# Kernel tuning notes

Hardware: AMD Instinct MI355X
Metric: run time of the kernel (lower is better)

The kernel has to match this reference:

```python
import jax, jax.numpy as jnp
import numpy as np

N_KEEP = 256      # number of retained DCT coefficients per box
MASK_LEN = 128    # reconstructed square mask side (gt_mask_len)
TOPK = 50         # boxes kept per image


def _zigzag_order(n):
    # order[i] = flat index (r*n+c) where the i-th zigzag element lives (JPEG zigzag)
    order = []
    for s in range(2 * n - 1):
        if s % 2 == 0:
            rng = range(min(s, n - 1), max(0, s - n + 1) - 1, -1)
        else:
            rng = range(max(0, s - n + 1), min(s, n - 1) + 1)
        for r in rng:
            order.append(r * n + (s - r))
    return np.asarray(order, dtype=np.int64)


def _dct_matrix(n):
    # orthonormal DCT-II matrix D; cv2.idct(Y) == D.T @ Y @ D
    k = np.arange(n)[:, None].astype(np.float64)
    m = np.arange(n)[None, :].astype(np.float64)
    D = np.cos(np.pi * (2.0 * m + 1.0) * k / (2.0 * n)) * np.sqrt(2.0 / n)
    D[0] *= np.sqrt(0.5)
    return D.astype(np.float32)

_INV_ZZ = np.argsort(_zigzag_order(MASK_LEN))  # flat[j] = padded_vec[_INV_ZZ[j]]
_DCT = _dct_matrix(MASK_LEN)


def setup_inputs() -> dict:
    key = jax.random.key(0)
    ks = jax.random.split(key, 6)
    B, Q, C, A = 32, 300, 91, 10
    return {
        "out_logits": jax.random.normal(ks[0], (B, Q, C), jnp.float32),
        "out_bbox": jax.random.uniform(ks[1], (B, Q, 4), jnp.float32),
        "out_vector": jax.random.normal(ks[2], (B, Q, N_KEEP), jnp.float32),
        "out_interms": jax.random.normal(ks[3], (B, Q, C), jnp.float32),
        "out_actions": jax.random.normal(ks[4], (B, 1, A), jnp.float32),
        "target_sizes": jax.random.randint(ks[5], (B, 2), 480, 1333, jnp.int32),
    }


def _box_cxcywh_to_xyxy(b):
    cx, cy, w, h = jnp.split(b, 4, axis=-1)
    return jnp.concatenate([cx - 0.5 * w, cy - 0.5 * h, cx + 0.5 * w, cy + 0.5 * h], axis=-1)


def reference(out_logits, out_bbox, out_vector, out_interms, out_actions, target_sizes):
    B, Q, C = out_logits.shape
    prob = jax.nn.sigmoid(out_logits)
    topk_values, topk_indexes = jax.lax.top_k(prob.reshape(B, -1), TOPK)
    scores = topk_values
    topk_boxes = topk_indexes // C          # [B, TOPK] query ids
    labels = topk_indexes % C               # [B, TOPK]

    boxes = _box_cxcywh_to_xyxy(out_bbox)
    boxes = jnp.take_along_axis(boxes, topk_boxes[:, :, None], axis=1)  # [B, TOPK, 4]

    prob_interms = jax.nn.sigmoid(out_interms)
    si = jnp.take_along_axis(prob_interms, topk_boxes[:, :, None], axis=1)  # [B, TOPK, C_int]
    labels_interms = jnp.argmax(si, axis=2)
    scores_interms = jnp.max(si, axis=2)

    prob_actions = jax.nn.softmax(out_actions[:, 0, :], axis=1)
    labels_action = jnp.argmax(prob_actions, axis=1)

    vectors = jnp.take_along_axis(out_vector, topk_boxes[:, :, None], axis=1)  # [B, TOPK, N_KEEP]

    ts = target_sizes.astype(boxes.dtype)
    img_h, img_w = ts[:, 0], ts[:, 1]
    scale_fct = jnp.stack([img_w, img_h, img_w, img_h], axis=1)
    boxes = boxes * scale_fct[:, None, :]

    # --- batched inverse zigzag + 2D IDCT + midpoint threshold ---
    pad = MASK_LEN * MASK_LEN - N_KEEP
    padded = jnp.pad(vectors, ((0, 0), (0, 0), (0, pad)))           # [B,TOPK,L*L]
    flat = padded[..., jnp.asarray(_INV_ZZ)]                         # inverse zigzag (gather)
    blocks = flat.reshape(B, TOPK, MASK_LEN, MASK_LEN)
    D = jnp.asarray(_DCT)
    re_mask = jnp.einsum('kn,bqkl,lm->bqnm', D, blocks, D)           # cv2.idct per box
    mx = jnp.max(re_mask, axis=(-2, -1), keepdims=True)
    mn = jnp.min(re_mask, axis=(-2, -1), keepdims=True)
    masks = (re_mask > 0.5 * (mx + mn)).astype(jnp.float32)          # [B,TOPK,L,L]

    return (scores, labels, boxes, masks, scores_interms, labels_interms, labels_action)
```

## Files before the change

kernel.cpp:

```cpp
#include <hip/hip_runtime.h>
#include <math.h>

#define BB 32
#define QQ 300
#define CC 91
#define TOPK 50
#define NKEEP 256
#define ML 128
#define QC (QQ * CC)
#define QC4 (QC / 4)
#define NWAVE 16
#define NSLICE 8
#define SL4 854
#define CAP 2048

#define OFF_SCORES ((size_t)0)
#define OFF_LABELS ((size_t)1600)
#define OFF_BOXES  ((size_t)3200)
#define OFF_MASKS  ((size_t)9600)
#define OFF_SI     ((size_t)26224000)
#define OFF_LI     ((size_t)26225600)
#define OFF_LA     ((size_t)26227200)

__device__ __forceinline__ uint32_t fkey(float f) {
    uint32_t u = __float_as_uint(f);
    return (u >> 31) ? ~u : (u | 0x80000000u);
}

__device__ __forceinline__ void pick_boundary(const uint32_t* bins, int kth, int lane,
                                              uint32_t* sBin, int* sNeed, int* sCnt) {
    uint4 h4 = *(const uint4*)&bins[lane * 4];
    uint32_t s3 = h4.w;
    uint32_t s2 = h4.z + s3;
    uint32_t s1 = h4.y + s2;
    uint32_t s0 = h4.x + s1;
    uint32_t inc = s0;
#pragma unroll
    for (int off = 1; off < 64; off <<= 1) {
        uint32_t v = __shfl_down(inc, off);
        if (lane + off < 64) inc += v;
    }
    uint32_t higher = inc - s0;
    uint32_t sarr[4] = {s0, s1, s2, s3};
    uint32_t harr[4] = {h4.x, h4.y, h4.z, h4.w};
#pragma unroll
    for (int c = 0; c < 4; ++c) {
        int cge = (int)(sarr[c] + higher);
        int cgt = cge - (int)harr[c];
        if (cge >= kth && cgt < kth) {
            *sBin = (uint32_t)(lane * 4 + c);
            *sNeed = kth - cgt;
            *sCnt = (int)harr[c];
        }
    }
}

__global__ __launch_bounds__(256) void topk_hist(const float* __restrict__ logits,
                                                 float* __restrict__ wsD,
                                                 int* __restrict__ wsZZ,
                                                 uint32_t* __restrict__ wsH) {
    int s = blockIdx.x;
    int b = blockIdx.y;
    int t = threadIdx.x;

    if (b == 0) {
        int lo = s * 368, hi = lo + 368;
        if (hi > 23 * 128) hi = 23 * 128;
        for (int idx = lo + t; idx < hi; idx += 256) {
            int k = idx >> 7, m = idx & 127;
            double v = cos((M_PI * (2.0 * (double)m + 1.0) * (double)k) / 256.0) * 0.125;
            if (k == 0) v *= sqrt(0.5);
            wsD[idx] = (float)v;
        }
        if (s == 0) {
            int j = t;
            int ss = 0;
            while ((ss + 1) * (ss + 2) / 2 <= j) ++ss;
            int o = j - ss * (ss + 1) / 2;
            int r = (ss & 1) ? o : (ss - o);
            int c = ss - r;
            wsZZ[j] = (r << 5) | c;
        }
    }

    __shared__ uint32_t hw[4 * 256];
    for (int i = t; i < 4 * 256; i += 256) hw[i] = 0;
    __syncthreads();

    uint32_t* myh = &hw[(t >> 6) * 256];
    const float4* base4 = (const float4*)(logits + (size_t)b * QC);
    int lo4 = s * SL4;
    int hi4 = lo4 + SL4; if (hi4 > QC4) hi4 = QC4;
    for (int p4 = lo4 + t; p4 < hi4; p4 += 256) {
        float4 v = base4[p4];
        atomicAdd(&myh[fkey(v.x) >> 24], 1u);
        atomicAdd(&myh[fkey(v.y) >> 24], 1u);
        atomicAdd(&myh[fkey(v.z) >> 24], 1u);
        atomicAdd(&myh[fkey(v.w) >> 24], 1u);
    }
    __syncthreads();

    if (t < 256) {
        uint32_t sum = hw[t] + hw[256 + t] + hw[512 + t] + hw[768 + t];
        wsH[((size_t)(b * NSLICE + s)) * 256 + t] = sum;
    }
}

__global__ __launch_bounds__(1024) void topk_select(const float* __restrict__ logits,
                                                    const float* __restrict__ bbox,
                                                    const float* __restrict__ actions,
                                                    const int* __restrict__ tsz,
                                                    float* __restrict__ out,
                                                    int* __restrict__ wsQ,
                                                    const uint32_t* __restrict__ wsH) {
    int b = blockIdx.x;
    int t = threadIdx.x;
    int lane = t & 63, w = t >> 6;

    __shared__ uint32_t histw[NWAVE * 256];
    __shared__ __attribute__((aligned(16))) uint32_t h2[256];
    __shared__ __attribute__((aligned(16))) uint32_t scn[256];
    __shared__ uint32_t sP;
    __shared__ int      sNeed, sCnt;
    __shared__ uint32_t cKey[TOPK];
    __shared__ int      cIdx[TOPK];
    __shared__ int      cntTop, cntN, cntE, sMin;
    __shared__ uint32_t candK[2][CAP];
    __shared__ int      candI[2][CAP];

    const float4* base4 = (const float4*)(logits + (size_t)b * QC);

    if (t < 256) {
        uint32_t ssum = 0;
#pragma unroll
        for (int s = 0; s < NSLICE; ++s) ssum += wsH[((size_t)(b * NSLICE + s)) * 256 + t];
        scn[t] = ssum;
    }
    if (t == 0) { cntTop = 0; cntN = 0; cntE = 0; }
    __syncthreads();
    if (t < 64) pick_boundary(scn, TOPK, lane, &sP, &sNeed, &sCnt);
    __syncthreads();
    uint32_t P0 = sP << 24;
    int need = sNeed;
    int nC0 = sCnt;

    if (nC0 <= CAP) {
        for (int p4 = t; p4 < QC4; p4 += 1024) {
            float4 v = base4[p4];
            uint32_t kk[4] = {fkey(v.x), fkey(v.y), fkey(v.z), fkey(v.w)};
#pragma unroll
            for (int c = 0; c < 4; ++c) {
                uint32_t hb = kk[c] & 0xFF000000u;
                if (hb > P0) {
                    int pos = atomicAdd(&cntTop, 1);
                    cKey[pos] = kk[c]; cIdx[pos] = 4 * p4 + c;
                } else if (hb == P0) {
                    int pos = atomicAdd(&cntN, 1);
                    candK[0][pos] = kk[c]; candI[0][pos] = 4 * p4 + c;
                }
            }
        }
        __syncthreads();
        int nc = cntN;
        int cur = 0;

        for (int level = 1; level <= 3; ++level) {
            if (nc <= need) break;
            int shift = 24 - 8 * level;
            if (t < 256) h2[t] = 0;
            if (t == 0) cntN = 0;
            __syncthreads();
            for (int j2 = t; j2 < nc; j2 += 1024)
                atomicAdd(&h2[(candK[cur][j2] >> shift) & 255u], 1u);
            __syncthreads();
            if (t < 64) pick_boundary(h2, need, lane, &sP, &sNeed, &sCnt);
            __syncthreads();
            uint32_t sub = sP;
            int needN = sNeed;
            for (int j2 = t; j2 < nc; j2 += 1024) {
                uint32_t k2 = candK[cur][j2]; int i2 = candI[cur][j2];
                uint32_t sb = (k2 >> shift) & 255u;
                if (sb > sub) {
                    int pos = atomicAdd(&cntTop, 1);
                    cKey[pos] = k2; cIdx[pos] = i2;
                } else if (sb == sub) {
                    int pos = atomicAdd(&cntN, 1);
                    candK[cur ^ 1][pos] = k2; candI[cur ^ 1][pos] = i2;
                }
            }
            __syncthreads();
            nc = cntN; need = needN; cur ^= 1;
        }

        int base = cntTop;
        if (nc <= need) {
            for (int j2 = t; j2 < nc; j2 += 1024) {
                cKey[base + j2] = candK[cur][j2];
                cIdx[base + j2] = candI[cur][j2];
            }
        } else {
            for (int j2 = t; j2 < nc; j2 += 1024) {
                int my = candI[cur][j2];
                int rank = 0;
                for (int m = 0; m < nc; ++m) rank += (candI[cur][m] < my);
                if (rank < need) { cKey[base + rank] = candK[cur][j2]; cIdx[base + rank] = my; }
            }
        }
        __syncthreads();
    } else {
        uint32_t Pfull = P0;
        int kth = need;
        uint32_t* myh = &histw[w * 256];
        for (int pass = 1; pass < 4; ++pass) {
            int shift = 24 - 8 * pass;
            for (int i2 = t; i2 < NWAVE * 256; i2 += 1024) histw[i2] = 0;
            __syncthreads();
            uint32_t pmask = 0xFFFFFFFFu << (shift + 8);
            for (int p4 = t; p4 < QC4; p4 += 1024) {
                float4 v = base4[p4];
                uint32_t kk[4] = {fkey(v.x), fkey(v.y), fkey(v.z), fkey(v.w)};
#pragma unroll
                for (int c = 0; c < 4; ++c)
                    if ((kk[c] & pmask) == Pfull) atomicAdd(&myh[(kk[c] >> shift) & 255u], 1u);
            }
            __syncthreads();
            if (t < 256) {
                uint32_t ssum = 0;
#pragma unroll
                for (int ww = 0; ww < NWAVE; ++ww) ssum += histw[ww * 256 + t];
                scn[t] = ssum;
            }
            __syncthreads();
            if (t < 64) pick_boundary(scn, kth, lane, &sP, &sNeed, &sCnt);
            __syncthreads();
            Pfull |= (sP << shift);
            kth = sNeed;
        }
        if (t == 0) { cntTop = 0; cntE = 0; }
        __syncthreads();
        for (int p4 = t; p4 < QC4; p4 += 1024) {
            float4 v = base4[p4];
            uint32_t kk[4] = {fkey(v.x), fkey(v.y), fkey(v.z), fkey(v.w)};
#pragma unroll
            for (int c = 0; c < 4; ++c) {
                if (kk[c] > Pfull) {
                    int pos = atomicAdd(&cntTop, 1);
                    cKey[pos] = kk[c]; cIdx[pos] = 4 * p4 + c;
                } else if (kk[c] == Pfull) {
                    int pos = atomicAdd(&cntE, 1);
                    if (pos < CAP) candI[0][pos] = 4 * p4 + c;
                }
            }
        }
        __syncthreads();
        int cgt2 = cntTop;
        int ne = cntE;
        if (ne <= CAP) {
            for (int j2 = t; j2 < ne; j2 += 1024) {
                int my = candI[0][j2];
                int rank = 0;
                for (int m = 0; m < ne; ++m) rank += (candI[0][m] < my);
                if (rank < kth) { cKey[cgt2 + rank] = Pfull; cIdx[cgt2 + rank] = my; }
            }
            __syncthreads();
        } else {
            int prevMin = -1;
            for (int r = 0; r < kth; ++r) {
                if (t == 0) sMin = 0x7fffffff;
                __syncthreads();
                int loc = 0x7fffffff;
                for (int p4 = t; p4 < QC4; p4 += 1024) {
                    float4 v = base4[p4];
                    uint32_t kk[4] = {fkey(v.x), fkey(v.y), fkey(v.z), fkey(v.w)};
#pragma unroll
                    for (int c = 0; c < 4; ++c) {
                        int idx = 4 * p4 + c;
                        if (kk[c] == Pfull && idx > prevMin) loc = min(loc, idx);
                    }
                }
                atomicMin(&sMin, loc);
                __syncthreads();
                prevMin = sMin;
                if (t == 0) { cKey[cgt2 + r] = Pfull; cIdx[cgt2 + r] = prevMin; }
                __syncthreads();
            }
        }
    }

    if (t < TOPK) {
        uint32_t myk = cKey[t]; int myi = cIdx[t];
        int rank = 0;
        for (int m = 0; m < TOPK; ++m) {
            uint32_t ok = cKey[m]; int oi = cIdx[m];
            rank += (ok > myk) || (ok == myk && oi < myi);
        }
        uint32_t u = (myk >> 31) ? (myk & 0x7fffffffu) : ~myk;
        float val = __uint_as_float(u);
        int q = myi / CC;
        int label = myi - q * CC;
        out[OFF_SCORES + b * TOPK + rank] = 1.0f / (1.0f + expf(-val));
        out[OFF_LABELS + b * TOPK + rank] = (float)label;
        wsQ[b * TOPK + rank] = q;
        const float* bbp = bbox + ((size_t)(b * QQ + q)) * 4;
        float cx = bbp[0], cy = bbp[1], bw = bbp[2], bh = bbp[3];
        float ih = (float)tsz[b * 2 + 0];
        float iw = (float)tsz[b * 2 + 1];
        float* bo = out + OFF_BOXES + ((size_t)(b * TOPK + rank)) * 4;
        bo[0] = (cx - 0.5f * bw) * iw;
        bo[1] = (cy - 0.5f * bh) * ih;
        bo[2] = (cx + 0.5f * bw) * iw;
        bo[3] = (cy + 0.5f * bh) * ih;
    }
    if (t == 0) {
        const float* ap = actions + (size_t)b * 10;
        float bv = ap[0]; int bi = 0;
        for (int i = 1; i < 10; ++i) { if (ap[i] > bv) { bv = ap[i]; bi = i; } }
        out[OFF_LA + b] = (float)bi;
    }
}

__global__ __launch_bounds__(256) void mask_kernel(const float* __restrict__ vec,
                                                   const float* __restrict__ interms,
                                                   const int* __restrict__ wsQ,
                                                   const float* __restrict__ wsD,
                                                   const int* __restrict__ wsZZ,
                                                   float* __restrict__ out) {
    int j = blockIdx.x;
    int b = blockIdx.y;
    int t = threadIdx.x;

    __shared__ float sT[23 * 128];
    __shared__ float sB[23 * 24];
    __shared__ float redv[4];
    __shared__ int   redi[4];
    __shared__ float redmn[4], redmx[4];

    int q = wsQ[b * TOPK + j];

    for (int i = t; i < 23 * 24; i += 256) sB[i] = 0.0f;
    __syncthreads();

    {
        int kl = wsZZ[t];
        float x = vec[((size_t)(b * QQ + q)) * NKEEP + t];
        sB[(kl >> 5) * 24 + (kl & 31)] = x;
    }

    int lane = t & 63, w = t >> 6;
    {
        float x = (t < CC) ? interms[((size_t)(b * QQ + q)) * CC + t] : -INFINITY;
        int xi = (t < CC) ? t : 0x7fffffff;
#pragma unroll
        for (int off = 32; off >= 1; off >>= 1) {
            float ov = __shfl_down(x, off);
            int   oi = __shfl_down(xi, off);
            bool better = (ov > x) || (ov == x && oi < xi);
            x = better ? ov : x;
            xi = better ? oi : xi;
        }
        if (lane == 0) { redv[w] = x; redi[w] = xi; }
    }
    __syncthreads();

    if (t == 0) {
        float gv = redv[0]; int gi = redi[0];
        for (int k = 1; k < 4; ++k) {
            bool better = (redv[k] > gv) || (redv[k] == gv && redi[k] < gi);
            gv = better ? redv[k] : gv;
            gi = better ? redi[k] : gi;
        }
        out[OFF_SI + (size_t)b * TOPK + j] = 1.0f / (1.0f + expf(-gv));
        out[OFF_LI + (size_t)b * TOPK + j] = (float)gi;
    }

    {
        int n = t & 127, h = t >> 7;
        float Dn[23];
#pragma unroll
        for (int k = 0; k < 23; ++k) Dn[k] = wsD[k * 128 + n];
#define S1L(L) { float a1 = 0.0f; \
    _Pragma("unroll") \
    for (int k = 0; k <= 22 - (L); ++k) a1 += Dn[k] * sB[k * 24 + (L)]; \
    sT[(L) * 128 + n] = a1; }
        if (h == 0) {
            S1L(0) S1L(2) S1L(4) S1L(6) S1L(8) S1L(10)
            S1L(12) S1L(14) S1L(16) S1L(18) S1L(20) S1L(22)
        } else {
            S1L(1) S1L(3) S1L(5) S1L(7) S1L(9) S1L(11)
            S1L(13) S1L(15) S1L(17) S1L(19) S1L(21)
        }
#undef S1L
    }
    __syncthreads();

    int tr = t >> 4, tc = t & 15;
    float acc[8][8];
#pragma unroll
    for (int a = 0; a < 8; ++a)
#pragma unroll
        for (int c = 0; c < 8; ++c) acc[a][c] = 0.0f;

#pragma unroll 4
    for (int l = 0; l < 23; ++l) {
        const float4 Ta = *(const float4*)&sT[l * 128 + tr * 8];
        const float4 Tb = *(const float4*)&sT[l * 128 + tr * 8 + 4];
        const float4 Da = *(const float4*)&wsD[l * 128 + tc * 8];
        const float4 Db = *(const float4*)&wsD[l * 128 + tc * 8 + 4];
        float Tv[8] = {Ta.x, Ta.y, Ta.z, Ta.w, Tb.x, Tb.y, Tb.z, Tb.w};
        float Dv[8] = {Da.x, Da.y, Da.z, Da.w, Db.x, Db.y, Db.z, Db.w};
#pragma unroll
        for (int a = 0; a < 8; ++a)
#pragma unroll
            for (int c = 0; c < 8; ++c) acc[a][c] += Tv[a] * Dv[c];
    }

    float mn = acc[0][0], mx = acc[0][0];
#pragma unroll
    for (int a = 0; a < 8; ++a)
#pragma unroll
        for (int c = 0; c < 8; ++c) {
            mn = fminf(mn, acc[a][c]);
            mx = fmaxf(mx, acc[a][c]);
        }
#pragma unroll
    for (int off = 32; off >= 1; off >>= 1) {
        mn = fminf(mn, __shfl_down(mn, off));
        mx = fmaxf(mx, __shfl_down(mx, off));
    }
    if (lane == 0) { redmn[w] = mn; redmx[w] = mx; }
    __syncthreads();
    float gmn = fminf(fminf(redmn[0], redmn[1]), fminf(redmn[2], redmn[3]));
    float gmx = fmaxf(fmaxf(redmx[0], redmx[1]), fmaxf(redmx[2], redmx[3]));
    float thr = 0.5f * (gmx + gmn);

    size_t bse = OFF_MASKS + ((size_t)(b * TOPK + j)) * 16384 + (size_t)tc * 8;
#pragma unroll
    for (int a = 0; a < 8; ++a) {
        int n = tr * 8 + a;
        float4 w0 = make_float4(acc[a][0] > thr ? 1.0f : 0.0f,
                                acc[a][1] > thr ? 1.0f : 0.0f,
                                acc[a][2] > thr ? 1.0f : 0.0f,
                                acc[a][3] > thr ? 1.0f : 0.0f);
        float4 w1 = make_float4(acc[a][4] > thr ? 1.0f : 0.0f,
                                acc[a][5] > thr ? 1.0f : 0.0f,
                                acc[a][6] > thr ? 1.0f : 0.0f,
                                acc[a][7] > thr ? 1.0f : 0.0f);
        *(float4*)&out[bse + (size_t)n * 128]     = w0;
        *(float4*)&out[bse + (size_t)n * 128 + 4] = w1;
    }
}

extern "C" void kernel_launch(void* const* d_in, const int* in_sizes, int n_in,
                              void* d_out, int out_size, void* d_ws, size_t ws_size,
                              hipStream_t stream) {
    const float* logits  = (const float*)d_in[0];
    const float* bbox    = (const float*)d_in[1];
    const float* vec     = (const float*)d_in[2];
    const float* interms = (const float*)d_in[3];
    const float* actions = (const float*)d_in[4];
    const int*   tsz     = (const int*)d_in[5];
    float* out = (float*)d_out;

    float*    wsD  = (float*)d_ws;
    int*      wsZZ = (int*)(wsD + 2944);
    int*      wsQ  = wsZZ + 256;
    uint32_t* wsH  = (uint32_t*)(wsQ + 1600);

    hipLaunchKernelGGL(topk_hist, dim3(NSLICE, BB), dim3(256), 0, stream,
                       logits, wsD, wsZZ, wsH);
    hipLaunchKernelGGL(topk_select, dim3(BB), dim3(1024), 0, stream,
                       logits, bbox, actions, tsz, out, wsQ, wsH);
    hipLaunchKernelGGL(mask_kernel, dim3(TOPK, BB), dim3(256), 0, stream,
                       vec, interms, wsQ, wsD, wsZZ, out);
}
```

Baseline: 163.3 us.

## Fuse top-k selection and mask reconstruction into one kernel with redundant per-block selection

Replaces the three-kernel pipeline (histogram, select, mask) with a single kernel launched over (TOPK, B). Every block redundantly recomputes the full top-k selection for its image and keeps only the entry whose rank equals its block index. The DCT table and zigzag map are now built in shared memory per block instead of read from workspace, and shared memory is reused through a union. This removes two launch boundaries and the global workspace round-trips. In exchange, the 109K-element logit scan and radix selection are repeated 50 times per image with only 256 threads per block, and the candidate capacity shrinks, so the slower fallback path may be taken more often.

```diff
diff --git a/kernel.cpp b/kernel.cpp
--- a/kernel.cpp
+++ b/kernel.cpp
@@ -6,13 +6,10 @@
 #define CC 91
 #define TOPK 50
 #define NKEEP 256
-#define ML 128
 #define QC (QQ * CC)
 #define QC4 (QC / 4)
-#define NWAVE 16
-#define NSLICE 8
-#define SL4 854
-#define CAP 2048
+#define NT 256
+#define CAP 1024
 
 #define OFF_SCORES ((size_t)0)
 #define OFF_LABELS ((size_t)1600)
@@ -55,97 +52,68 @@
     }
 }
 
-__global__ __launch_bounds__(256) void topk_hist(const float* __restrict__ logits,
-                                                 float* __restrict__ wsD,
-                                                 int* __restrict__ wsZZ,
-                                                 uint32_t* __restrict__ wsH) {
-    int s = blockIdx.x;
+union alignas(16) Smem {
+    struct {
+        uint32_t hw[4 * 256];
+        uint32_t scn[256];
+        uint32_t h2[256];
+        uint32_t candK[2][CAP];
+        int      candI[2][CAP];
+        uint32_t cKey[TOPK];
+        int      cIdx[TOPK];
+    } s;
+    struct {
+        float sD[23 * 128];
+        float sT[23 * 128];
+        float sB[23 * 24];
+        int   sZZ[256];
+        float redv[4]; int redi[4];
+        float redmn[4], redmx[4];
+    } m;
+};
+
+__global__ __launch_bounds__(NT) void fused_all(const float* __restrict__ logits,
+                                                const float* __restrict__ bbox,
+                                                const float* __restrict__ vec,
+                                                const float* __restrict__ interms,
+                                                const float* __restrict__ actions,
+                                                const int* __restrict__ tsz,
+                                                float* __restrict__ out) {
+    int j = blockIdx.x;
     int b = blockIdx.y;
     int t = threadIdx.x;
-
-    if (b == 0) {
-        int lo = s * 368, hi = lo + 368;
-        if (hi > 23 * 128) hi = 23 * 128;
-        for (int idx = lo + t; idx < hi; idx += 256) {
-            int k = idx >> 7, m = idx & 127;
-            double v = cos((M_PI * (2.0 * (double)m + 1.0) * (double)k) / 256.0) * 0.125;
-            if (k == 0) v *= sqrt(0.5);
-            wsD[idx] = (float)v;
-        }
-        if (s == 0) {
-            int j = t;
-            int ss = 0;
-            while ((ss + 1) * (ss + 2) / 2 <= j) ++ss;
-            int o = j - ss * (ss + 1) / 2;
-            int r = (ss & 1) ? o : (ss - o);
-            int c = ss - r;
-            wsZZ[j] = (r << 5) | c;
-        }
-    }
-
-    __shared__ uint32_t hw[4 * 256];
-    for (int i = t; i < 4 * 256; i += 256) hw[i] = 0;
-    __syncthreads();
-
-    uint32_t* myh = &hw[(t >> 6) * 256];
+    int lane = t & 63, w4 = t >> 6;
+
+    __shared__ Smem sm;
+    __shared__ uint32_t sP;
+    __shared__ int sNeed, sCnt, cntTop, cntN, cntE, sMin, sQ;
+
     const float4* base4 = (const float4*)(logits + (size_t)b * QC);
-    int lo4 = s * SL4;
-    int hi4 = lo4 + SL4; if (hi4 > QC4) hi4 = QC4;
-    for (int p4 = lo4 + t; p4 < hi4; p4 += 256) {
-        float4 v = base4[p4];
-        atomicAdd(&myh[fkey(v.x) >> 24], 1u);
-        atomicAdd(&myh[fkey(v.y) >> 24], 1u);
-        atomicAdd(&myh[fkey(v.z) >> 24], 1u);
-        atomicAdd(&myh[fkey(v.w) >> 24], 1u);
-    }
-    __syncthreads();
-
-    if (t < 256) {
-        uint32_t sum = hw[t] + hw[256 + t] + hw[512 + t] + hw[768 + t];
-        wsH[((size_t)(b * NSLICE + s)) * 256 + t] = sum;
-    }
-}
-
-__global__ __launch_bounds__(1024) void topk_select(const float* __restrict__ logits,
-                                                    const float* __restrict__ bbox,
-                                                    const float* __restrict__ actions,
-                                                    const int* __restrict__ tsz,
-                                                    float* __restrict__ out,
-                                                    int* __restrict__ wsQ,
-                                                    const uint32_t* __restrict__ wsH) {
-    int b = blockIdx.x;
-    int t = threadIdx.x;
-    int lane = t & 63, w = t >> 6;
-
-    __shared__ uint32_t histw[NWAVE * 256];
-    __shared__ __attribute__((aligned(16))) uint32_t h2[256];
-    __shared__ __attribute__((aligned(16))) uint32_t scn[256];
-    __shared__ uint32_t sP;
-    __shared__ int      sNeed, sCnt;
-    __shared__ uint32_t cKey[TOPK];
-    __shared__ int      cIdx[TOPK];
-    __shared__ int      cntTop, cntN, cntE, sMin;
-    __shared__ uint32_t candK[2][CAP];
-    __shared__ int      candI[2][CAP];
-
-    const float4* base4 = (const float4*)(logits + (size_t)b * QC);
-
-    if (t < 256) {
-        uint32_t ssum = 0;
-#pragma unroll
-        for (int s = 0; s < NSLICE; ++s) ssum += wsH[((size_t)(b * NSLICE + s)) * 256 + t];
-        scn[t] = ssum;
-    }
+
+    for (int i = t; i < 4 * 256; i += NT) sm.s.hw[i] = 0;
+    __syncthreads();
+    {
+        uint32_t* myh = &sm.s.hw[w4 * 256];
+        for (int p4 = t; p4 < QC4; p4 += NT) {
+            float4 v = base4[p4];
+            atomicAdd(&myh[fkey(v.x) >> 24], 1u);
+            atomicAdd(&myh[fkey(v.y) >> 24], 1u);
+            atomicAdd(&myh[fkey(v.z) >> 24], 1u);
+            atomicAdd(&myh[fkey(v.w) >> 24], 1u);
+        }
+    }
+    __syncthreads();
+    if (t < 256) sm.s.scn[t] = sm.s.hw[t] + sm.s.hw[256 + t] + sm.s.hw[512 + t] + sm.s.hw[768 + t];
     if (t == 0) { cntTop = 0; cntN = 0; cntE = 0; }
     __syncthreads();
-    if (t < 64) pick_boundary(scn, TOPK, lane, &sP, &sNeed, &sCnt);
+    if (t < 64) pick_boundary(sm.s.scn, TOPK, lane, &sP, &sNeed, &sCnt);
     __syncthreads();
     uint32_t P0 = sP << 24;
     int need = sNeed;
     int nC0 = sCnt;
 
     if (nC0 <= CAP) {
-        for (int p4 = t; p4 < QC4; p4 += 1024) {
+        for (int p4 = t; p4 < QC4; p4 += NT) {
             float4 v = base4[p4];
             uint32_t kk[4] = {fkey(v.x), fkey(v.y), fkey(v.z), fkey(v.w)};
 #pragma unroll
@@ -153,39 +121,38 @@
                 uint32_t hb = kk[c] & 0xFF000000u;
                 if (hb > P0) {
                     int pos = atomicAdd(&cntTop, 1);
-                    cKey[pos] = kk[c]; cIdx[pos] = 4 * p4 + c;
+                    sm.s.cKey[pos] = kk[c]; sm.s.cIdx[pos] = 4 * p4 + c;
                 } else if (hb == P0) {
                     int pos = atomicAdd(&cntN, 1);
-                    candK[0][pos] = kk[c]; candI[0][pos] = 4 * p4 + c;
+                    sm.s.candK[0][pos] = kk[c]; sm.s.candI[0][pos] = 4 * p4 + c;
                 }
             }
         }
         __syncthreads();
-        int nc = cntN;
-        int cur = 0;
+        int nc = cntN, cur = 0;
 
         for (int level = 1; level <= 3; ++level) {
             if (nc <= need) break;
             int shift = 24 - 8 * level;
-            if (t < 256) h2[t] = 0;
+            if (t < 256) sm.s.h2[t] = 0;
             if (t == 0) cntN = 0;
             __syncthreads();
-            for (int j2 = t; j2 < nc; j2 += 1024)
-                atomicAdd(&h2[(candK[cur][j2] >> shift) & 255u], 1u);
-            __syncthreads();
-            if (t < 64) pick_boundary(h2, need, lane, &sP, &sNeed, &sCnt);
+            for (int j2 = t; j2 < nc; j2 += NT)
+                atomicAdd(&sm.s.h2[(sm.s.candK[cur][j2] >> shift) & 255u], 1u);
+            __syncthreads();
+            if (t < 64) pick_boundary(sm.s.h2, need, lane, &sP, &sNeed, &sCnt);
             __syncthreads();
             uint32_t sub = sP;
             int needN = sNeed;
-            for (int j2 = t; j2 < nc; j2 += 1024) {
-                uint32_t k2 = candK[cur][j2]; int i2 = candI[cur][j2];
+            for (int j2 = t; j2 < nc; j2 += NT) {
+                uint32_t k2 = sm.s.candK[cur][j2]; int i2 = sm.s.candI[cur][j2];
                 uint32_t sb = (k2 >> shift) & 255u;
                 if (sb > sub) {
                     int pos = atomicAdd(&cntTop, 1);
-                    cKey[pos] = k2; cIdx[pos] = i2;
+                    sm.s.cKey[pos] = k2; sm.s.cIdx[pos] = i2;
                 } else if (sb == sub) {
                     int pos = atomicAdd(&cntN, 1);
-                    candK[cur ^ 1][pos] = k2; candI[cur ^ 1][pos] = i2;
+                    sm.s.candK[cur ^ 1][pos] = k2; sm.s.candI[cur ^ 1][pos] = i2;
                 }
             }
             __syncthreads();
@@ -194,29 +161,29 @@
 
         int base = cntTop;
         if (nc <= need) {
-            for (int j2 = t; j2 < nc; j2 += 1024) {
-                cKey[base + j2] = candK[cur][j2];
-                cIdx[base + j2] = candI[cur][j2];
+            for (int j2 = t; j2 < nc; j2 += NT) {
+                sm.s.cKey[base + j2] = sm.s.candK[cur][j2];
+                sm.s.cIdx[base + j2] = sm.s.candI[cur][j2];
             }
         } else {
-            for (int j2 = t; j2 < nc; j2 += 1024) {
-                int my = candI[cur][j2];
+            for (int j2 = t; j2 < nc; j2 += NT) {
+                int my = sm.s.candI[cur][j2];
                 int rank = 0;
-                for (int m = 0; m < nc; ++m) rank += (candI[cur][m] < my);
-                if (rank < need) { cKey[base + rank] = candK[cur][j2]; cIdx[base + rank] = my; }
+                for (int m = 0; m < nc; ++m) rank += (sm.s.candI[cur][m] < my);
+                if (rank < need) { sm.s.cKey[base + rank] = sm.s.candK[cur][j2]; sm.s.cIdx[base + rank] = my; }
             }
         }
         __syncthreads();
     } else {
         uint32_t Pfull = P0;
         int kth = need;
-        uint32_t* myh = &histw[w * 256];
+        uint32_t* myh = &sm.s.hw[w4 * 256];
         for (int pass = 1; pass < 4; ++pass) {
             int shift = 24 - 8 * pass;
-            for (int i2 = t; i2 < NWAVE * 256; i2 += 1024) histw[i2] = 0;
+            for (int i2 = t; i2 < 4 * 256; i2 += NT) sm.s.hw[i2] = 0;
             __syncthreads();
             uint32_t pmask = 0xFFFFFFFFu << (shift + 8);
-            for (int p4 = t; p4 < QC4; p4 += 1024) {
+            for (int p4 = t; p4 < QC4; p4 += NT) {
                 float4 v = base4[p4];
                 uint32_t kk[4] = {fkey(v.x), fkey(v.y), fkey(v.z), fkey(v.w)};
 #pragma unroll
@@ -224,31 +191,26 @@
                     if ((kk[c] & pmask) == Pfull) atomicAdd(&myh[(kk[c] >> shift) & 255u], 1u);
             }
             __syncthreads();
-            if (t < 256) {
-                uint32_t ssum = 0;
-#pragma unroll
-                for (int ww = 0; ww < NWAVE; ++ww) ssum += histw[ww * 256 + t];
-                scn[t] = ssum;
-            }
-            __syncthreads();
-            if (t < 64) pick_boundary(scn, kth, lane, &sP, &sNeed, &sCnt);
+            if (t < 256) sm.s.scn[t] = sm.s.hw[t] + sm.s.hw[256 + t] + sm.s.hw[512 + t] + sm.s.hw[768 + t];
+            __syncthreads();
+            if (t < 64) pick_boundary(sm.s.scn, kth, lane, &sP, &sNeed, &sCnt);
             __syncthreads();
             Pfull |= (sP << shift);
             kth = sNeed;
         }
         if (t == 0) { cntTop = 0; cntE = 0; }
         __syncthreads();
-        for (int p4 = t; p4 < QC4; p4 += 1024) {
+        for (int p4 = t; p4 < QC4; p4 += NT) {
             float4 v = base4[p4];
             uint32_t kk[4] = {fkey(v.x), fkey(v.y), fkey(v.z), fkey(v.w)};
 #pragma unroll
             for (int c = 0; c < 4; ++c) {
                 if (kk[c] > Pfull) {
                     int pos = atomicAdd(&cntTop, 1);
-                    cKey[pos] = kk[c]; cIdx[pos] = 4 * p4 + c;
+                    sm.s.cKey[pos] = kk[c]; sm.s.cIdx[pos] = 4 * p4 + c;
                 } else if (kk[c] == Pfull) {
                     int pos = atomicAdd(&cntE, 1);
-                    if (pos < CAP) candI[0][pos] = 4 * p4 + c;
+                    if (pos < CAP) sm.s.candI[0][pos] = 4 * p4 + c;
                 }
             }
         }
@@ -256,11 +218,11 @@
         int cgt2 = cntTop;
         int ne = cntE;
         if (ne <= CAP) {
-            for (int j2 = t; j2 < ne; j2 += 1024) {
-                int my = candI[0][j2];
+            for (int j2 = t; j2 < ne; j2 += NT) {
+                int my = sm.s.candI[0][j2];
                 int rank = 0;
-                for (int m = 0; m < ne; ++m) rank += (candI[0][m] < my);
-                if (rank < kth) { cKey[cgt2 + rank] = Pfull; cIdx[cgt2 + rank] = my; }
+                for (int m = 0; m < ne; ++m) rank += (sm.s.candI[0][m] < my);
+                if (rank < kth) { sm.s.cKey[cgt2 + rank] = Pfull; sm.s.cIdx[cgt2 + rank] = my; }
             }
             __syncthreads();
         } else {
@@ -269,7 +231,7 @@
                 if (t == 0) sMin = 0x7fffffff;
                 __syncthreads();
                 int loc = 0x7fffffff;
-                for (int p4 = t; p4 < QC4; p4 += 1024) {
+                for (int p4 = t; p4 < QC4; p4 += NT) {
                     float4 v = base4[p4];
                     uint32_t kk[4] = {fkey(v.x), fkey(v.y), fkey(v.z), fkey(v.w)};
 #pragma unroll
@@ -281,72 +243,71 @@
                 atomicMin(&sMin, loc);
                 __syncthreads();
                 prevMin = sMin;
-                if (t == 0) { cKey[cgt2 + r] = Pfull; cIdx[cgt2 + r] = prevMin; }
+                if (t == 0) { sm.s.cKey[cgt2 + r] = Pfull; sm.s.cIdx[cgt2 + r] = prevMin; }
                 __syncthreads();
             }
         }
     }
 
     if (t < TOPK) {
-        uint32_t myk = cKey[t]; int myi = cIdx[t];
+        uint32_t myk = sm.s.cKey[t]; int myi = sm.s.cIdx[t];
         int rank = 0;
         for (int m = 0; m < TOPK; ++m) {
-            uint32_t ok = cKey[m]; int oi = cIdx[m];
+            uint32_t ok = sm.s.cKey[m]; int oi = sm.s.cIdx[m];
             rank += (ok > myk) || (ok == myk && oi < myi);
         }
-        uint32_t u = (myk >> 31) ? (myk & 0x7fffffffu) : ~myk;
-        float val = __uint_as_float(u);
-        int q = myi / CC;
-        int label = myi - q * CC;
-        out[OFF_SCORES + b * TOPK + rank] = 1.0f / (1.0f + expf(-val));
-        out[OFF_LABELS + b * TOPK + rank] = (float)label;
-        wsQ[b * TOPK + rank] = q;
-        const float* bbp = bbox + ((size_t)(b * QQ + q)) * 4;
-        float cx = bbp[0], cy = bbp[1], bw = bbp[2], bh = bbp[3];
-        float ih = (float)tsz[b * 2 + 0];
-        float iw = (float)tsz[b * 2 + 1];
-        float* bo = out + OFF_BOXES + ((size_t)(b * TOPK + rank)) * 4;
-        bo[0] = (cx - 0.5f * bw) * iw;
-        bo[1] = (cy - 0.5f * bh) * ih;
-        bo[2] = (cx + 0.5f * bw) * iw;
-        bo[3] = (cy + 0.5f * bh) * ih;
-    }
-    if (t == 0) {
+        if (rank == j) {
+            uint32_t u = (myk >> 31) ? (myk & 0x7fffffffu) : ~myk;
+            float val = __uint_as_float(u);
+            int q = myi / CC;
+            int label = myi - q * CC;
+            out[OFF_SCORES + b * TOPK + j] = 1.0f / (1.0f + expf(-val));
+            out[OFF_LABELS + b * TOPK + j] = (float)label;
+            const float* bbp = bbox + ((size_t)(b * QQ + q)) * 4;
+            float cx = bbp[0], cy = bbp[1], bw = bbp[2], bh = bbp[3];
+            float ih = (float)tsz[b * 2 + 0];
+            float iw = (float)tsz[b * 2 + 1];
+            float* bo = out + OFF_BOXES + ((size_t)(b * TOPK + j)) * 4;
+            bo[0] = (cx - 0.5f * bw) * iw;
+            bo[1] = (cy - 0.5f * bh) * ih;
+            bo[2] = (cx + 0.5f * bw) * iw;
+            bo[3] = (cy + 0.5f * bh) * ih;
+            sQ = q;
+        }
+    }
+    if (j == 0 && t == 0) {
         const float* ap = actions + (size_t)b * 10;
         float bv = ap[0]; int bi = 0;
         for (int i = 1; i < 10; ++i) { if (ap[i] > bv) { bv = ap[i]; bi = i; } }
         out[OFF_LA + b] = (float)bi;
     }
-}
-
-__global__ __launch_bounds__(256) void mask_kernel(const float* __restrict__ vec,
-                                                   const float* __restrict__ interms,
-                                                   const int* __restrict__ wsQ,
-                                                   const float* __restrict__ wsD,
-                                                   const int* __restrict__ wsZZ,
-                                                   float* __restrict__ out) {
-    int j = blockIdx.x;
-    int b = blockIdx.y;
-    int t = threadIdx.x;
-
-    __shared__ float sT[23 * 128];
-    __shared__ float sB[23 * 24];
-    __shared__ float redv[4];
-    __shared__ int   redi[4];
-    __shared__ float redmn[4], redmx[4];
-
-    int q = wsQ[b * TOPK + j];
-
-    for (int i = t; i < 23 * 24; i += 256) sB[i] = 0.0f;
-    __syncthreads();
-
+    __syncthreads();
+    int q = sQ;
+
+    for (int idx = t; idx < 23 * 128; idx += NT) {
+        int k = idx >> 7, m = idx & 127;
+        double v = cos((M_PI * (2.0 * (double)m + 1.0) * (double)k) / 256.0) * 0.125;
+        if (k == 0) v *= sqrt(0.5);
+        sm.m.sD[idx] = (float)v;
+    }
     {
-        int kl = wsZZ[t];
+        int jj = t;
+        int ss = 0;
+        while ((ss + 1) * (ss + 2) / 2 <= jj) ++ss;
+        int o = jj - ss * (ss + 1) / 2;
+        int r = (ss & 1) ? o : (ss - o);
+        int ccol = ss - r;
+        sm.m.sZZ[t] = (r << 5) | ccol;
+    }
+    for (int i = t; i < 23 * 24; i += NT) sm.m.sB[i] = 0.0f;
+    __syncthreads();
+
+    {
+        int kl = sm.m.sZZ[t];
         float x = vec[((size_t)(b * QQ + q)) * NKEEP + t];
-        sB[(kl >> 5) * 24 + (kl & 31)] = x;
-    }
-
-    int lane = t & 63, w = t >> 6;
+        sm.m.sB[(kl >> 5) * 24 + (kl & 31)] = x;
+    }
+
     {
         float x = (t < CC) ? interms[((size_t)(b * QQ + q)) * CC + t] : -INFINITY;
         int xi = (t < CC) ? t : 0x7fffffff;
@@ -358,16 +319,16 @@
             x = better ? ov : x;
             xi = better ? oi : xi;
         }
-        if (lane == 0) { redv[w] = x; redi[w] = xi; }
+        if (lane == 0) { sm.m.redv[w4] = x; sm.m.redi[w4] = xi; }
     }
     __syncthreads();
 
     if (t == 0) {
-        float gv = redv[0]; int gi = redi[0];
+        float gv = sm.m.redv[0]; int gi = sm.m.redi[0];
         for (int k = 1; k < 4; ++k) {
-            bool better = (redv[k] > gv) || (redv[k] == gv && redi[k] < gi);
-            gv = better ? redv[k] : gv;
-            gi = better ? redi[k] : gi;
+            bool better = (sm.m.redv[k] > gv) || (sm.m.redv[k] == gv && sm.m.redi[k] < gi);
+            gv = better ? sm.m.redv[k] : gv;
+            gi = better ? sm.m.redi[k] : gi;
         }
         out[OFF_SI + (size_t)b * TOPK + j] = 1.0f / (1.0f + expf(-gv));
         out[OFF_LI + (size_t)b * TOPK + j] = (float)gi;
@@ -377,11 +338,11 @@
         int n = t & 127, h = t >> 7;
         float Dn[23];
 #pragma unroll
-        for (int k = 0; k < 23; ++k) Dn[k] = wsD[k * 128 + n];
+        for (int k = 0; k < 23; ++k) Dn[k] = sm.m.sD[k * 128 + n];
 #define S1L(L) { float a1 = 0.0f; \
     _Pragma("unroll") \
-    for (int k = 0; k <= 22 - (L); ++k) a1 += Dn[k] * sB[k * 24 + (L)]; \
-    sT[(L) * 128 + n] = a1; }
+    for (int k = 0; k <= 22 - (L); ++k) a1 += Dn[k] * sm.m.sB[k * 24 + (L)]; \
+    sm.m.sT[(L) * 128 + n] = a1; }
         if (h == 0) {
             S1L(0) S1L(2) S1L(4) S1L(6) S1L(8) S1L(10)
             S1L(12) S1L(14) S1L(16) S1L(18) S1L(20) S1L(22)
@@ -402,10 +363,10 @@
 
 #pragma unroll 4
     for (int l = 0; l < 23; ++l) {
-        const float4 Ta = *(const float4*)&sT[l * 128 + tr * 8];
-        const float4 Tb = *(const float4*)&sT[l * 128 + tr * 8 + 4];
-        const float4 Da = *(const float4*)&wsD[l * 128 + tc * 8];
-        const float4 Db = *(const float4*)&wsD[l * 128 + tc * 8 + 4];
+        const float4 Ta = *(const float4*)&sm.m.sT[l * 128 + tr * 8];
+        const float4 Tb = *(const float4*)&sm.m.sT[l * 128 + tr * 8 + 4];
+        const float4 Da = *(const float4*)&sm.m.sD[l * 128 + tc * 8];
+        const float4 Db = *(const float4*)&sm.m.sD[l * 128 + tc * 8 + 4];
         float Tv[8] = {Ta.x, Ta.y, Ta.z, Ta.w, Tb.x, Tb.y, Tb.z, Tb.w};
         float Dv[8] = {Da.x, Da.y, Da.z, Da.w, Db.x, Db.y, Db.z, Db.w};
 #pragma unroll
@@ -427,10 +388,10 @@
         mn = fminf(mn, __shfl_down(mn, off));
         mx = fmaxf(mx, __shfl_down(mx, off));
     }
-    if (lane == 0) { redmn[w] = mn; redmx[w] = mx; }
-    __syncthreads();
-    float gmn = fminf(fminf(redmn[0], redmn[1]), fminf(redmn[2], redmn[3]));
-    float gmx = fmaxf(fmaxf(redmx[0], redmx[1]), fmaxf(redmx[2], redmx[3]));
+    if (lane == 0) { sm.m.redmn[w4] = mn; sm.m.redmx[w4] = mx; }
+    __syncthreads();
+    float gmn = fminf(fminf(sm.m.redmn[0], sm.m.redmn[1]), fminf(sm.m.redmn[2], sm.m.redmn[3]));
+    float gmx = fmaxf(fmaxf(sm.m.redmx[0], sm.m.redmx[1]), fmaxf(sm.m.redmx[2], sm.m.redmx[3]));
     float thr = 0.5f * (gmx + gmn);
 
     size_t bse = OFF_MASKS + ((size_t)(b * TOPK + j)) * 16384 + (size_t)tc * 8;
@@ -461,15 +422,6 @@
     const int*   tsz     = (const int*)d_in[5];
     float* out = (float*)d_out;
 
-    float*    wsD  = (float*)d_ws;
-    int*      wsZZ = (int*)(wsD + 2944);
-    int*      wsQ  = wsZZ + 256;
-    uint32_t* wsH  = (uint32_t*)(wsQ + 1600);
-
-    hipLaunchKernelGGL(topk_hist, dim3(NSLICE, BB), dim3(256), 0, stream,
-                       logits, wsD, wsZZ, wsH);
-    hipLaunchKernelGGL(topk_select, dim3(BB), dim3(1024), 0, stream,
-                       logits, bbox, actions, tsz, out, wsQ, wsH);
-    hipLaunchKernelGGL(mask_kernel, dim3(TOPK, BB), dim3(256), 0, stream,
-                       vec, interms, wsQ, wsD, wsZZ, out);
+    hipLaunchKernelGGL(fused_all, dim3(TOPK, BB), dim3(NT), 0, stream,
+                       logits, bbox, vec, interms, actions, tsz, out);
 }
```

Result: slower. 266.2 us (+63.0%).

## Fuse top-k histogram kernel into select kernel and shrink candidate buffer

Applied to the files above, without the earlier changes.

Removes the separate topk_hist launch and builds the first-byte histogram inside topk_select, one 1024-thread block per image, using per-wave shared histograms. DCT matrix and zigzag table generation move into the first blocks of the select kernel. This saves a kernel launch and the global round trip of partial histograms, at the cost of less parallelism (32 blocks instead of 256) for the histogram pass. CAP is halved to 1024 to cut shared memory, which may send more inputs down the slower full-rescan path.

```diff
diff --git a/kernel.cpp b/kernel.cpp
--- a/kernel.cpp
+++ b/kernel.cpp
@@ -6,13 +6,10 @@
 #define CC 91
 #define TOPK 50
 #define NKEEP 256
-#define ML 128
 #define QC (QQ * CC)
 #define QC4 (QC / 4)
 #define NWAVE 16
-#define NSLICE 8
-#define SL4 854
-#define CAP 2048
+#define CAP 1024
 
 #define OFF_SCORES ((size_t)0)
 #define OFF_LABELS ((size_t)1600)
@@ -55,24 +52,28 @@
     }
 }
 
-__global__ __launch_bounds__(256) void topk_hist(const float* __restrict__ logits,
-                                                 float* __restrict__ wsD,
-                                                 int* __restrict__ wsZZ,
-                                                 uint32_t* __restrict__ wsH) {
-    int s = blockIdx.x;
-    int b = blockIdx.y;
+__global__ __launch_bounds__(1024) void topk_select(const float* __restrict__ logits,
+                                                    const float* __restrict__ bbox,
+                                                    const float* __restrict__ actions,
+                                                    const int* __restrict__ tsz,
+                                                    float* __restrict__ out,
+                                                    int* __restrict__ wsQ,
+                                                    float* __restrict__ wsD,
+                                                    int* __restrict__ wsZZ) {
+    int b = blockIdx.x;
     int t = threadIdx.x;
-
-    if (b == 0) {
-        int lo = s * 368, hi = lo + 368;
+    int lane = t & 63, w = t >> 6;
+
+    if (b < 8) {
+        int lo = b * 368, hi = lo + 368;
         if (hi > 23 * 128) hi = 23 * 128;
-        for (int idx = lo + t; idx < hi; idx += 256) {
+        for (int idx = lo + t; idx < hi; idx += 1024) {
             int k = idx >> 7, m = idx & 127;
             double v = cos((M_PI * (2.0 * (double)m + 1.0) * (double)k) / 256.0) * 0.125;
             if (k == 0) v *= sqrt(0.5);
             wsD[idx] = (float)v;
         }
-        if (s == 0) {
+        if (b == 0 && t < NKEEP) {
             int j = t;
             int ss = 0;
             while ((ss + 1) * (ss + 2) / 2 <= j) ++ss;
@@ -83,43 +84,9 @@
         }
     }
 
-    __shared__ uint32_t hw[4 * 256];
-    for (int i = t; i < 4 * 256; i += 256) hw[i] = 0;
-    __syncthreads();
-
-    uint32_t* myh = &hw[(t >> 6) * 256];
-    const float4* base4 = (const float4*)(logits + (size_t)b * QC);
-    int lo4 = s * SL4;
-    int hi4 = lo4 + SL4; if (hi4 > QC4) hi4 = QC4;
-    for (int p4 = lo4 + t; p4 < hi4; p4 += 256) {
-        float4 v = base4[p4];
-        atomicAdd(&myh[fkey(v.x) >> 24], 1u);
-        atomicAdd(&myh[fkey(v.y) >> 24], 1u);
-        atomicAdd(&myh[fkey(v.z) >> 24], 1u);
-        atomicAdd(&myh[fkey(v.w) >> 24], 1u);
-    }
-    __syncthreads();
-
-    if (t < 256) {
-        uint32_t sum = hw[t] + hw[256 + t] + hw[512 + t] + hw[768 + t];
-        wsH[((size_t)(b * NSLICE + s)) * 256 + t] = sum;
-    }
-}
-
-__global__ __launch_bounds__(1024) void topk_select(const float* __restrict__ logits,
-                                                    const float* __restrict__ bbox,
-                                                    const float* __restrict__ actions,
-                                                    const int* __restrict__ tsz,
-                                                    float* __restrict__ out,
-                                                    int* __restrict__ wsQ,
-                                                    const uint32_t* __restrict__ wsH) {
-    int b = blockIdx.x;
-    int t = threadIdx.x;
-    int lane = t & 63, w = t >> 6;
-
-    __shared__ uint32_t histw[NWAVE * 256];
+    __shared__ uint32_t hw[NWAVE * 256];
+    __shared__ __attribute__((aligned(16))) uint32_t scn[256];
     __shared__ __attribute__((aligned(16))) uint32_t h2[256];
-    __shared__ __attribute__((aligned(16))) uint32_t scn[256];
     __shared__ uint32_t sP;
     __shared__ int      sNeed, sCnt;
     __shared__ uint32_t cKey[TOPK];
@@ -130,13 +97,26 @@
 
     const float4* base4 = (const float4*)(logits + (size_t)b * QC);
 
+    for (int i = t; i < NWAVE * 256; i += 1024) hw[i] = 0;
+    if (t == 0) { cntTop = 0; cntN = 0; cntE = 0; }
+    __syncthreads();
+    {
+        uint32_t* myh = &hw[w * 256];
+        for (int p4 = t; p4 < QC4; p4 += 1024) {
+            float4 v = base4[p4];
+            atomicAdd(&myh[fkey(v.x) >> 24], 1u);
+            atomicAdd(&myh[fkey(v.y) >> 24], 1u);
+            atomicAdd(&myh[fkey(v.z) >> 24], 1u);
+            atomicAdd(&myh[fkey(v.w) >> 24], 1u);
+        }
+    }
+    __syncthreads();
     if (t < 256) {
-        uint32_t ssum = 0;
-#pragma unroll
-        for (int s = 0; s < NSLICE; ++s) ssum += wsH[((size_t)(b * NSLICE + s)) * 256 + t];
-        scn[t] = ssum;
-    }
-    if (t == 0) { cntTop = 0; cntN = 0; cntE = 0; }
+        uint32_t s = 0;
+#pragma unroll
+        for (int ww = 0; ww < NWAVE; ++ww) s += hw[ww * 256 + t];
+        scn[t] = s;
+    }
     __syncthreads();
     if (t < 64) pick_boundary(scn, TOPK, lane, &sP, &sNeed, &sCnt);
     __syncthreads();
@@ -161,8 +141,7 @@
             }
         }
         __syncthreads();
-        int nc = cntN;
-        int cur = 0;
+        int nc = cntN, cur = 0;
 
         for (int level = 1; level <= 3; ++level) {
             if (nc <= need) break;
@@ -210,10 +189,10 @@
     } else {
         uint32_t Pfull = P0;
         int kth = need;
-        uint32_t* myh = &histw[w * 256];
+        uint32_t* myh = &hw[w * 256];
         for (int pass = 1; pass < 4; ++pass) {
             int shift = 24 - 8 * pass;
-            for (int i2 = t; i2 < NWAVE * 256; i2 += 1024) histw[i2] = 0;
+            for (int i2 = t; i2 < NWAVE * 256; i2 += 1024) hw[i2] = 0;
             __syncthreads();
             uint32_t pmask = 0xFFFFFFFFu << (shift + 8);
             for (int p4 = t; p4 < QC4; p4 += 1024) {
@@ -227,7 +206,7 @@
             if (t < 256) {
                 uint32_t ssum = 0;
 #pragma unroll
-                for (int ww = 0; ww < NWAVE; ++ww) ssum += histw[ww * 256 + t];
+                for (int ww = 0; ww < NWAVE; ++ww) ssum += hw[ww * 256 + t];
                 scn[t] = ssum;
             }
             __syncthreads();
@@ -461,15 +440,12 @@
     const int*   tsz     = (const int*)d_in[5];
     float* out = (float*)d_out;
 
-    float*    wsD  = (float*)d_ws;
-    int*      wsZZ = (int*)(wsD + 2944);
-    int*      wsQ  = wsZZ + 256;
-    uint32_t* wsH  = (uint32_t*)(wsQ + 1600);
-
-    hipLaunchKernelGGL(topk_hist, dim3(NSLICE, BB), dim3(256), 0, stream,
-                       logits, wsD, wsZZ, wsH);
+    float* wsD  = (float*)d_ws;
+    int*   wsZZ = (int*)(wsD + 2944);
+    int*   wsQ  = wsZZ + 256;
+
     hipLaunchKernelGGL(topk_select, dim3(BB), dim3(1024), 0, stream,
-                       logits, bbox, actions, tsz, out, wsQ, wsH);
+                       logits, bbox, actions, tsz, out, wsQ, wsD, wsZZ);
     hipLaunchKernelGGL(mask_kernel, dim3(TOPK, BB), dim3(256), 0, stream,
                        vec, interms, wsQ, wsD, wsZZ, out);
 }
```

Result: no change. 165.7 us (median of 2 runs) (+1.5%).
